# Kernel tuning notes

Measured on AMD Instinct MI355X. Metric: run time of the kernel, lower is better.

Reference implementation:

```python
import jax, jax.numpy as jnp
import numpy as np

B, F_IN, N_D, N_A, VBS, N_STEPS = 1024, 256, 64, 64, 128, 3
FO = N_D + N_A            # 128
D_CAT = 2 * F_IN          # 512
AD = F_IN                 # attention_dim = 256
GAMMA, EPSILON, BN_EPS = 1.3, 1e-15, 1e-5
SQRT_HALF = 0.7071067811865476


def _bn(x, w, b):
    # full-batch BatchNorm1d (training mode, biased var)
    m = x.mean(0)
    v = x.var(0)
    return (x - m) / jnp.sqrt(v + BN_EPS) * w + b


def _gbn(x, w, b):
    # Ghost BatchNorm: per virtual-batch statistics
    n, f = x.shape
    xr = x.reshape(n // VBS, VBS, f)
    m = xr.mean(1, keepdims=True)
    v = xr.var(1, keepdims=True)
    return (xr - m).reshape(n, f) / jnp.sqrt(v + BN_EPS).repeat(VBS, axis=0).reshape(n, f) * w + b


def _glu(x, fcw, bnw, bnb):
    h = _gbn(x @ fcw.T, bnw, bnb)
    d = h.shape[-1] // 2
    return h[:, :d] * jax.nn.sigmoid(h[:, d:])


def _feat_transformer(x, fc0, bnw0, bnb0, fc1, bnw1, bnb1):
    # independent GLU block, first=True, n_glu_independent=2
    h = _glu(x, fc0, bnw0, bnb0)
    return (h + _glu(h, fc1, bnw1, bnb1)) * SQRT_HALF


def _sparsemax(z):
    f = z.shape[-1]
    zs = -jnp.sort(-z, axis=-1)                      # descending
    k = jnp.arange(1, f + 1, dtype=z.dtype)
    zc = jnp.cumsum(zs, axis=-1)
    support = (1.0 + k * zs) > zc
    kz = jnp.sum(support, axis=-1, keepdims=True)
    tau = (jnp.take_along_axis(zc, kz - 1, axis=-1) - 1.0) / kz.astype(z.dtype)
    return jnp.maximum(z - tau, 0.0)


def _self_attn_1d(x, in_w, in_b, out_w, out_b):
    # nn.MultiheadAttention(embed_dim=1, heads=1) over the feature axis
    q = x * in_w[0] + in_b[0]
    k = x * in_w[1] + in_b[1]
    v = x * in_w[2] + in_b[2]
    attn = jax.nn.softmax(jnp.einsum('bi,bj->bij', q, k), axis=-1)  # scale 1/sqrt(1)
    y = jnp.einsum('bij,bj->bi', attn, v) * out_w + out_b
    return y, attn


def setup_inputs() -> dict:
    key = jax.random.key(0)
    ks = iter(jax.random.split(key, 32))
    s = 0.1
    d = {
        'x': jax.random.normal(next(ks), (B, F_IN), jnp.float32),
        'bemv': jax.random.normal(next(ks), (B, F_IN), jnp.float32),
        'gmat': jax.random.uniform(next(ks), (AD, F_IN), jnp.float32),
        'bn_w': jnp.ones((F_IN,), jnp.float32),
        'bn_b': jnp.zeros((F_IN,), jnp.float32),
        'init_fc0': jax.random.normal(next(ks), (2 * FO, D_CAT), jnp.float32) * s,
        'init_bnw0': jnp.ones((2 * FO,), jnp.float32),
        'init_bnb0': jnp.zeros((2 * FO,), jnp.float32),
        'init_fc1': jax.random.normal(next(ks), (2 * FO, FO), jnp.float32) * s,
        'init_bnw1': jnp.ones((2 * FO,), jnp.float32),
        'init_bnb1': jnp.zeros((2 * FO,), jnp.float32),
        'step_fc0': jax.random.normal(next(ks), (N_STEPS, 2 * FO, D_CAT), jnp.float32) * s,
        'step_bnw0': jnp.ones((N_STEPS, 2 * FO), jnp.float32),
        'step_bnb0': jnp.zeros((N_STEPS, 2 * FO), jnp.float32),
        'step_fc1': jax.random.normal(next(ks), (N_STEPS, 2 * FO, FO), jnp.float32) * s,
        'step_bnw1': jnp.ones((N_STEPS, 2 * FO), jnp.float32),
        'step_bnb1': jnp.zeros((N_STEPS, 2 * FO), jnp.float32),
        'att_fc': jax.random.normal(next(ks), (N_STEPS, AD, N_A), jnp.float32) * s,
        'att_bnw': jnp.ones((N_STEPS, AD), jnp.float32),
        'att_bnb': jnp.zeros((N_STEPS, AD), jnp.float32),
        'sa_in_w': jax.random.normal(next(ks), (N_STEPS, 3), jnp.float32),
        'sa_in_b': jnp.zeros((N_STEPS, 3), jnp.float32),
        'sa_out_w': jax.random.normal(next(ks), (N_STEPS,), jnp.float32),
        'sa_out_b': jnp.zeros((N_STEPS,), jnp.float32),
    }
    return d


def reference(x, bemv, gmat, bn_w, bn_b,
              init_fc0, init_bnw0, init_bnb0, init_fc1, init_bnw1, init_bnb1,
              step_fc0, step_bnw0, step_bnb0, step_fc1, step_bnw1, step_bnb1,
              att_fc, att_bnw, att_bnb,
              sa_in_w, sa_in_b, sa_out_w, sa_out_b):
    prior = jnp.ones((x.shape[0], AD), x.dtype)
    xn = _bn(x, bn_w, bn_b)
    x_cat = jnp.concatenate([xn, bemv], axis=1)
    feat_out = _feat_transformer(x_cat, init_fc0, init_bnw0, init_bnb0,
                                 init_fc1, init_bnw1, init_bnb1)
    att = feat_out[:, N_D:]
    m_loss = jnp.asarray(0.0, x.dtype)
    steps, amaps = [], []
    for s in range(N_STEPS):
        a = _gbn(att @ att_fc[s].T, att_bnw[s], att_bnb[s])
        tab_mask = _sparsemax(a * prior)
        m_loss = m_loss + jnp.mean(jnp.sum(tab_mask * jnp.log(tab_mask + EPSILON), axis=1))
        prior = prior * (GAMMA - tab_mask)
        x_masked = (tab_mask @ gmat) * xn
        x_masked, A = _self_attn_1d(x_masked, sa_in_w[s], sa_in_b[s], sa_out_w[s], sa_out_b[s])
        amaps.append(A)
        feat_out = _feat_transformer(jnp.concatenate([x_masked, bemv], axis=1),
                                     step_fc0[s], step_bnw0[s], step_bnb0[s],
                                     step_fc1[s], step_bnw1[s], step_bnb1[s])
        steps.append(jax.nn.leaky_relu(feat_out[:, :N_D], 0.01))
        att = feat_out[:, N_D:]
    m_loss = m_loss / N_STEPS
    return jnp.stack(steps), m_loss, jnp.stack(amaps)
```

## Files before the change

### kernel.cpp

```cpp
#include <hip/hip_runtime.h>
#include <hip/hip_bf16.h>

#define BATCH 1024
#define N_STEPS 3
#define GAMMA_C 1.3f
#define BN_EPS_C 1e-5f
#define SQRT_HALF_C 0.70710678118654752440f
#define ST_STRIDE 786432

__device__ __forceinline__ float ldin(const void* p, size_t i, int isbf){
  if (isbf) return __bfloat162float(((const __hip_bfloat16*)p)[i]);
  return ((const float*)p)[i];
}
__device__ __forceinline__ float4 ld4(const void* p, size_t i, int isbf){
  if (!isbf) return *(const float4*)((const float*)p + i);
  const __hip_bfloat16* q = (const __hip_bfloat16*)p + i;
  return make_float4(__bfloat162float(q[0]), __bfloat162float(q[1]),
                     __bfloat162float(q[2]), __bfloat162float(q[3]));
}

__device__ __forceinline__ float wsum(float v){
#pragma unroll
  for (int o = 32; o > 0; o >>= 1) v += __shfl_xor(v, o);
  return v;
// ... 38 lines not shown
  float k2 = kS[(cb+2) & 255];
  float k3 = kS[(cb+3) & 255];
  const bool cross = (cb == 255);
  const int nj = (t < 255) ? 64 : 63;
#pragma unroll 4
  for (int j = 0; j < nj; ++j){
    int r0 = 4*j + rb0;
    float q0 = sh[r0], m0 = sh[256+r0], z0 = sh[512+r0];
    float4 o;
    if (!cross){
      o.x = __expf(q0*k0 - m0) * z0;
      o.y = __expf(q0*k1 - m0) * z0;
      o.z = __expf(q0*k2 - m0) * z0;
      o.w = __expf(q0*k3 - m0) * z0;
    } else {
      float q1 = sh[r0+1], m1 = sh[256+r0+1], z1 = sh[512+r0+1];
      o.x = __expf(q0*k0 - m0) * z0;
      o.y = __expf(q1*k1 - m1) * z1;
      o.z = __expf(q1*k2 - m1) * z1;
      o.w = __expf(q1*k3 - m1) * z1;
    }
    *(float4*)(tp + 3 + 4*t + 1024*j) = o;
  }
  if (t == 0){
    float q0 = sh[0], m0 = sh[256], z0 = sh[512];
    tp[0] = __expf(q0*kS[0] - m0) * z0;
    tp[1] = __expf(q0*kS[1] - m0) * z0;
    tp[2] = __expf(q0*kS[2] - m0) * z0;
    float qL = sh[255], mL = sh[511], zL = sh[767];
    tp[65535] = __expf(qL*kS[255] - mL) * zL;
  }
}

__global__ void detect_k(const unsigned short* __restrict__ u, float* __restrict__ flag){
  __shared__ int cnt;
  if (threadIdx.x == 0) cnt = 0;
  __syncthreads();
  int c = 0;
  for (int j = 0; j < 16; ++j){
    unsigned short v = u[(size_t)(threadIdx.x * 16 + j) * 2];
    int e = (v >> 7) & 0xFF;
    if (e >= 118 && e <= 134) c++;
  }
  atomicAdd(&cnt, c);
  __syncthreads();
  if (threadIdx.x == 0) flag[0] = (cnt > 2048) ? 1.0f : 0.0f;
}

__global__ void bnstats_k(const void* __restrict__ x, float* __restrict__ mean,
                          float* __restrict__ istd, const float* __restrict__ flg){
  __shared__ float sb[256];
  const int isbf = flg[0] != 0.0f;
  int f = blockIdx.x, t = threadIdx.x;
  float s = 0.f, ss = 0.f;
  for (int r = t; r < BATCH; r += 256){
    float v = ldin(x, (size_t)r * 256 + f, isbf);
    s += v; ss += v * v;
  }
  s  = block_sum(s, sb);
  ss = block_sum(ss, sb);
  if (t == 0){
    float m = s * (1.f / BATCH);
    mean[f] = m;
    istd[f] = rsqrtf(ss * (1.f / BATCH) - m * m + BN_EPS_C);
  }
}

__global__ void xn_k(const void* __restrict__ x, const float* __restrict__ mean,
                     const float* __restrict__ istd, const void* __restrict__ bw,
                     const void* __restrict__ bb, float* __restrict__ xn,
                     const float* __restrict__ flg){
  const int isbf = flg[0] != 0.0f;
  int idx = blockIdx.x * 256 + threadIdx.x;
  int f = idx & 255;
  xn[idx] = (ldin(x, idx, isbf) - mean[f]) * istd[f] * ldin(bw, f, isbf) + ldin(bb, f, isbf);
}

__global__ __launch_bounds__(256)
void gemm_bt_k(const float* __restrict__ A1, const void* __restrict__ A2, int split,
               const void* __restrict__ W, size_t woff, float* __restrict__ C, int K,
               const float* __restrict__ st, float* __restrict__ amap, int dS, int dR0,
               const float* __restrict__ flg){
  int bid = blockIdx.x, t = threadIdx.x;
  if (bid >= 256){ drain_rows(st, amap, dS, dR0 + bid - 256, t); return; }
  __shared__ float As[32][34];
  __shared__ float Ws[32][34];
  const int isbf = flg[0] != 0.0f;
  const int n0 = (bid & 7) * 32, m0 = (bid >> 3) * 32;
  const int tx = t & 15, ty = t >> 4;
  const int lr = t >> 3, lk = (t & 7) * 4;
  const int nc = K >> 5;
  float a00 = 0.f, a01 = 0.f, a10 = 0.f, a11 = 0.f;

  auto lda = [&](int k0) -> float4 {
    int gk = k0 + lk, gr = m0 + lr;
    if (gk < split) return *(const float4*)(A1 + (size_t)gr * split + gk);
    return ld4(A2, (size_t)gr * (K - split) + (gk - split), isbf);
  };
  auto ldw = [&](int k0) -> float4 {
    return ld4(W, woff + (size_t)(n0 + lr) * K + k0 + lk, isbf);
  };

  float4 ra = lda(0), rw = ldw(0);
  for (int c = 0; c < nc; ++c){
    As[lk+0][lr] = ra.x; As[lk+1][lr] = ra.y; As[lk+2][lr] = ra.z; As[lk+3][lr] = ra.w;
    Ws[lk+0][lr] = rw.x; Ws[lk+1][lr] = rw.y; Ws[lk+2][lr] = rw.z; Ws[lk+3][lr] = rw.w;
    __syncthreads();
    float4 na = ra, nw = rw;
    if (c + 1 < nc){ na = lda((c+1) << 5); nw = ldw((c+1) << 5); }
#pragma unroll
    for (int kk = 0; kk < 32; ++kk){
      float2 av = *(const float2*)&As[kk][ty*2];
      float2 wv = *(const float2*)&Ws[kk][tx*2];
      a00 += av.x * wv.x; a01 += av.x * wv.y;
      a10 += av.y * wv.x; a11 += av.y * wv.y;
    }
    __syncthreads();
    ra = na; rw = nw;
  }
  int r0 = m0 + ty*2, c0 = n0 + tx*2;
  float* Cp = C + (size_t)r0 * 256 + c0;
  Cp[0] = a00; Cp[1] = a01; Cp[256] = a10; Cp[257] = a11;
}

__global__ __launch_bounds__(256)
void glugemm_k(const float* __restrict__ H1, const void* __restrict__ gw,
               const void* __restrict__ gb, size_t goff,
               const void* __restrict__ W, size_t woff, float* __restrict__ C,
               const float* __restrict__ st, float* __restrict__ amap, int dS, int dR0,
               const float* __restrict__ flg){
  int bid = blockIdx.x, t = threadIdx.x;
  if (bid >= 256){ drain_rows(st, amap, dS, dR0 + bid - 256, t); return; }
  __shared__ __align__(16) float sA[256], sB[256];
  __shared__ float As[32][34];
  __shared__ float Ws[32][34];
  const int isbf = flg[0] != 0.0f;
  const int n0 = (bid & 7) * 32, m0 = (bid >> 3) * 32;
  const int g = bid >> 5;
  {
    const float* Hp = H1 + (size_t)g*32768 + t;
    float s = 0.f, ss = 0.f;
#pragma unroll 8
    for (int i = 0; i < 128; ++i){ float v = Hp[(size_t)i*256]; s += v; ss += v*v; }
    float m = s * (1.f/128), is = rsqrtf(ss * (1.f/128) - m*m + BN_EPS_C);
    float wv = ldin(gw, goff + t, isbf), bv = ldin(gb, goff + t, isbf);
    float A = is * wv;
    sA[t] = A; sB[t] = bv - m*A;
  }
  __syncthreads();
  const int tx = t & 15, ty = t >> 4;
  const int lr = t >> 3, lk = (t & 7) * 4;
  float a00 = 0.f, a01 = 0.f, a10 = 0.f, a11 = 0.f;

  auto lda = [&](int k0) -> float4 {
    int gk = k0 + lk, gr = m0 + lr;
    const float* h = H1 + (size_t)gr*256;
    float4 h0 = *(const float4*)(h + gk);
    float4 h1 = *(const float4*)(h + gk + 128);
    float4 A0 = *(const float4*)(sA + gk);
    float4 B0 = *(const float4*)(sB + gk);
    float4 A1 = *(const float4*)(sA + gk + 128);
    float4 B1 = *(const float4*)(sB + gk + 128);
    float4 r;
    r.x = (h0.x*A0.x+B0.x) / (1.f + __expf(-(h1.x*A1.x+B1.x)));
    r.y = (h0.y*A0.y+B0.y) / (1.f + __expf(-(h1.y*A1.y+B1.y)));
    r.z = (h0.z*A0.z+B0.z) / (1.f + __expf(-(h1.z*A1.z+B1.z)));
    r.w = (h0.w*A0.w+B0.w) / (1.f + __expf(-(h1.w*A1.w+B1.w)));
    return r;
  };
  auto ldw = [&](int k0) -> float4 {
    return ld4(W, woff + (size_t)(n0 + lr) * 128 + k0 + lk, isbf);
  };

  float4 ra = lda(0), rw = ldw(0);
#pragma unroll 1
  for (int c = 0; c < 4; ++c){
    As[lk+0][lr] = ra.x; As[lk+1][lr] = ra.y; As[lk+2][lr] = ra.z; As[lk+3][lr] = ra.w;
    Ws[lk+0][lr] = rw.x; Ws[lk+1][lr] = rw.y; Ws[lk+2][lr] = rw.z; Ws[lk+3][lr] = rw.w;
    __syncthreads();
    float4 na = ra, nw = rw;
    if (c + 1 < 4){ na = lda((c+1) << 5); nw = ldw((c+1) << 5); }
#pragma unroll
    for (int kk = 0; kk < 32; ++kk){
      float2 av = *(const float2*)&As[kk][ty*2];
      float2 wv = *(const float2*)&Ws[kk][tx*2];
      a00 += av.x * wv.x; a01 += av.x * wv.y;
      a10 += av.y * wv.x; a11 += av.y * wv.y;
    }
    __syncthreads();
    ra = na; rw = nw;
  }
  int r0 = m0 + ty*2, c0 = n0 + tx*2;
  float* Cp = C + (size_t)r0 * 256 + c0;
  Cp[0] = a00; Cp[1] = a01; Cp[256] = a10; Cp[257] = a11;
}

__global__ __launch_bounds__(256)
void spmax_k(const float* __restrict__ Ha, const void* __restrict__ gw,
             const void* __restrict__ gb, size_t goff, float* __restrict__ prior,
             const float* __restrict__ xn, const void* __restrict__ gmat,
             float* __restrict__ xm, float* __restrict__ lrow, int first,
             const float* __restrict__ st, float* __restrict__ amap, int dS, int dR0,
             const float* __restrict__ flg){
  int bid = blockIdx.x, t = threadIdx.x;
  if (bid >= 256){ drain_rows(st, amap, dS, dR0 + bid - 256, t); return; }
  __shared__ __align__(16) float sAA[256], sBA[256];
  __shared__ __align__(16) float tabs[4][256];
  __shared__ unsigned int msk[4][2];
  const int isbf = flg[0] != 0.0f;
  const int g = bid >> 5;
  {
    const float* Hp = Ha + (size_t)g*32768 + t;
    float s = 0.f, ss = 0.f;
#pragma unroll 8
    for (int i = 0; i < 128; ++i){ float v = Hp[(size_t)i*256]; s += v; ss += v*v; }
    float m = s * (1.f/128), is = rsqrtf(ss * (1.f/128) - m*m + BN_EPS_C);
    float wv = ldin(gw, goff + t, isbf), bv = ldin(gb, goff + t, isbf);
    float A = is * wv;
    sAA[t] = A; sBA[t] = bv - m*A;
  }
  __syncthreads();
  int lane = t & 63, wv = t >> 6;
  int b0 = bid * 4;
  int b = b0 + wv;
  size_t rb = (size_t)b * 256;
  int j0 = lane * 4;
  float4 h4 = *(const float4*)(Ha + rb + j0);
  float4 A4 = *(const float4*)(sAA + j0);
  float4 B4 = *(const float4*)(sBA + j0);
  float pr[4];
  if (first){ pr[0] = pr[1] = pr[2] = pr[3] = 1.f; }
  else { float4 p4 = *(const float4*)(prior + rb + j0); pr[0]=p4.x; pr[1]=p4.y; pr[2]=p4.z; pr[3]=p4.w; }
  float z[4];
  z[0] = (h4.x*A4.x + B4.x) * pr[0];
  z[1] = (h4.y*A4.y + B4.y) * pr[1];
  z[2] = (h4.z*A4.z + B4.z) * pr[2];
  z[3] = (h4.w*A4.w + B4.w) * pr[3];
  float zm = wmaxr(fmaxf(fmaxf(z[0], z[1]), fmaxf(z[2], z[3])));
  float lo = zm - 1.f, hi = zm;
#pragma unroll 1
  for (int it = 0; it < 30; ++it){
    float mid = 0.5f * (lo + hi);
    float sv = 0.f;
#pragma unroll
    for (int e = 0; e < 4; ++e){ float d = z[e] - mid; sv += d > 0.f ? d : 0.f; }
    sv = wsum(sv);
    if (sv >= 1.f) lo = mid; else hi = mid;
  }
  float tau = 0.5f * (lo + hi);
  float p[4], ls = 0.f;
#pragma unroll
  for (int e = 0; e < 4; ++e){
    p[e] = z[e] - tau; p[e] = p[e] > 0.f ? p[e] : 0.f;
    ls += p[e] * __logf(p[e] + 1e-15f);
  }
  *(float4*)&tabs[wv][j0] = make_float4(p[0], p[1], p[2], p[3]);
  *(float4*)(prior + rb + j0) = make_float4(pr[0]*(GAMMA_C-p[0]), pr[1]*(GAMMA_C-p[1]),
                                            pr[2]*(GAMMA_C-p[2]), pr[3]*(GAMMA_C-p[3]));
  ls = wsum(ls);
  if (lane == 0) lrow[b] = ls;
  bool nz = (p[0] > 0.f) | (p[1] > 0.f) | (p[2] > 0.f) | (p[3] > 0.f);
  unsigned long long bm = __ballot(nz);
  if (lane == 0){ msk[wv][0] = (unsigned int)bm; msk[wv][1] = (unsigned int)(bm >> 32); }
  __syncthreads();
  unsigned long long M0 = msk[0][0] | ((unsigned long long)msk[0][1] << 32);
  unsigned long long M1 = msk[1][0] | ((unsigned long long)msk[1][1] << 32);
  unsigned long long M2 = msk[2][0] | ((unsigned long long)msk[2][1] << 32);
  unsigned long long M3 = msk[3][0] | ((unsigned long long)msk[3][1] << 32);
  float a0 = 0.f, a1 = 0.f, a2 = 0.f, a3 = 0.f;
#pragma unroll 1
  for (int c = 0; c < 64; ++c){
    int r0a = (int)((M0 >> c) & 1), r1a = (int)((M1 >> c) & 1);
    int r2a = (int)((M2 >> c) & 1), r3a = (int)((M3 >> c) & 1);
    if (r0a | r1a | r2a | r3a){
      int k = c * 4;
      float g0 = ldin(gmat, (size_t)(k+0)*256 + t, isbf);
      float g1 = ldin(gmat, (size_t)(k+1)*256 + t, isbf);
      float g2 = ldin(gmat, (size_t)(k+2)*256 + t, isbf);
      float g3 = ldin(gmat, (size_t)(k+3)*256 + t, isbf);
      if (r0a){ float4 tv = *(float4*)&tabs[0][k]; a0 += tv.x*g0 + tv.y*g1 + tv.z*g2 + tv.w*g3; }
      if (r1a){ float4 tv = *(float4*)&tabs[1][k]; a1 += tv.x*g0 + tv.y*g1 + tv.z*g2 + tv.w*g3; }
      if (r2a){ float4 tv = *(float4*)&tabs[2][k]; a2 += tv.x*g0 + tv.y*g1 + tv.z*g2 + tv.w*g3; }
      if (r3a){ float4 tv = *(float4*)&tabs[3][k]; a3 += tv.x*g0 + tv.y*g1 + tv.z*g2 + tv.w*g3; }
    }
  }
  xm[(size_t)(b0+0)*256 + t] = a0 * xn[(size_t)(b0+0)*256 + t];
  xm[(size_t)(b0+1)*256 + t] = a1 * xn[(size_t)(b0+1)*256 + t];
  xm[(size_t)(b0+2)*256 + t] = a2 * xn[(size_t)(b0+2)*256 + t];
  xm[(size_t)(b0+3)*256 + t] = a3 * xn[(size_t)(b0+3)*256 + t];
}

__global__ __launch_bounds__(256)
void attnA_k(const float* __restrict__ xm, float* __restrict__ y,
             const void* __restrict__ siw, const void* __restrict__ sib,
             const void* __restrict__ sow, const void* __restrict__ sob,
             int s, float* __restrict__ st, float* __restrict__ amap, int dS, int dR0,
             const float* __restrict__ flg){
  int bid = blockIdx.x, t = threadIdx.x;
  if (bid >= 1024){ drain_rows(st, amap, dS, dR0 + bid - 1024, t); return; }
  __shared__ __align__(16) float ks[256], vs[256];
  __shared__ float r1[4], r2[4];
  const int isbf = flg[0] != 0.0f;
  int b = bid;
  float w0 = ldin(siw, s*3+0, isbf), w1 = ldin(siw, s*3+1, isbf), w2 = ldin(siw, s*3+2, isbf);
  float b0 = ldin(sib, s*3+0, isbf), b1 = ldin(sib, s*3+1, isbf), b2 = ldin(sib, s*3+2, isbf);
  float ow = ldin(sow, s, isbf), ob = ldin(sob, s, isbf);
  float xv = xm[(size_t)b*256 + t];
  float q = xv*w0 + b0, k = xv*w1 + b1, v = xv*w2 + b2;
  ks[t] = k; vs[t] = v;
  int lane = t & 63, wv = t >> 6;
  float km = wmaxr(k), kn = wminr(k);
  if (lane == 0){ r1[wv] = km; r2[wv] = kn; }
  __syncthreads();
  float kmax = fmaxf(fmaxf(r1[0], r1[1]), fmaxf(r1[2], r1[3]));
  float kmin = fminf(fminf(r2[0], r2[1]), fminf(r2[2], r2[3]));
  float mi = (q >= 0.f) ? q*kmax : q*kmin;
  float Z = 0.f, Y = 0.f;
#pragma unroll 8
  for (int j = 0; j < 256; j += 4){
    float4 k4 = *(const float4*)&ks[j];
    float4 v4 = *(const float4*)&vs[j];
    float e0 = __expf(q*k4.x - mi), e1 = __expf(q*k4.y - mi);
    float e2 = __expf(q*k4.z - mi), e3 = __expf(q*k4.w - mi);
    Z += (e0 + e1) + (e2 + e3);
    Y += (e0*v4.x + e1*v4.y) + (e2*v4.z + e3*v4.w);
  }
  float rz = 1.f / Z;
  y[(size_t)b*256 + t] = Y*rz*ow + ob;
  size_t sb = ((size_t)s*BATCH + b)*256 + t;
  st[sb]               = q;
  st[ST_STRIDE + sb]   = k;
  st[2*ST_STRIDE + sb] = mi;
  st[3*ST_STRIDE + sb] = rz;
}

__global__ __launch_bounds__(256)
void comb_k(const float* __restrict__ H1, const void* __restrict__ pw0,
            const void* __restrict__ pb0, size_t off0,
            const float* __restrict__ H2, const void* __restrict__ pw1,
            const void* __restrict__ pb1, size_t off1,
            float* __restrict__ att, float* __restrict__ steps,
            const float* __restrict__ st, float* __restrict__ amap, int dS, int dR0,
            const float* __restrict__ flg){
  int bid = blockIdx.x, t = threadIdx.x;
  if (bid >= 512){ drain_rows(st, amap, dS, dR0 + bid - 512, t); return; }
  __shared__ float sA0[256], sB0[256], sA1[256], sB1[256];
  const int isbf = flg[0] != 0.0f;
  const int g = bid >> 6;
  {
    const float* Hp = H1 + (size_t)g*32768 + t;
    float s = 0.f, ss = 0.f;
#pragma unroll 8
    for (int i = 0; i < 128; ++i){ float v = Hp[(size_t)i*256]; s += v; ss += v*v; }
    float m = s * (1.f/128), is = rsqrtf(ss * (1.f/128) - m*m + BN_EPS_C);
    float wv = ldin(pw0, off0 + t, isbf), bv = ldin(pb0, off0 + t, isbf);
    float A = is * wv;
    sA0[t] = A; sB0[t] = bv - m*A;
  }
  {
    const float* Hp = H2 + (size_t)g*32768 + t;
    float s = 0.f, ss = 0.f;
#pragma unroll 8
    for (int i = 0; i < 128; ++i){ float v = Hp[(size_t)i*256]; s += v; ss += v*v; }
    float m = s * (1.f/128), is = rsqrtf(ss * (1.f/128) - m*m + BN_EPS_C);
    float wv = ldin(pw1, off1 + t, isbf), bv = ldin(pb1, off1 + t, isbf);
    float A = is * wv;
    sA1[t] = A; sB1[t] = bv - m*A;
  }
  __syncthreads();
  int r = bid*2 + (t >> 7), j = t & 127;
  float h0 = H1[(size_t)r*256 + j], h1 = H1[(size_t)r*256 + j + 128];
  float u0 = h0 * sA0[j]     + sB0[j];
  float u1 = h1 * sA0[j+128] + sB0[j+128];
  float g0 = u0 / (1.f + __expf(-u1));
  float v0 = H2[(size_t)r*256 + j]     * sA1[j]     + sB1[j];
  float v1 = H2[(size_t)r*256 + j+128] * sA1[j+128] + sB1[j+128];
  float g1 = v0 / (1.f + __expf(-v1));
  float f = (g0 + g1) * SQRT_HALF_C;
  if (j < 64){
    if (steps) steps[(size_t)r*64 + j] = f > 0.f ? f : 0.01f*f;
  } else {
    att[(size_t)r*64 + (j - 64)] = f;
  }
}

__global__ __launch_bounds__(256)
void mloss_k(const float* __restrict__ lrow, float* __restrict__ outp,
             const float* __restrict__ st, float* __restrict__ amap, int s, int row0){
  int bid = blockIdx.x, t = threadIdx.x;
  if (bid > 0){ drain_rows(st, amap, s, row0 + bid - 1, t); return; }
  __shared__ float sb[256];
  float v = 0.f;
  for (int i = t; i < N_STEPS*BATCH; i += 256) v += lrow[i];
  v = block_sum(v, sb);
  if (t == 0) outp[0] = v * (1.f/(N_STEPS*(float)BATCH));
}

extern "C" void kernel_launch(void* const* d_in, const int* in_sizes, int n_in,
                              void* d_out, int out_size, void* d_ws, size_t ws_size,
                              hipStream_t stream){
  const void* x         = d_in[0];
  const void* bemv      = d_in[1];
  const void* gmat      = d_in[2];
  const void* bn_w      = d_in[3];
  const void* bn_b      = d_in[4];
  const void* init_fc0  = d_in[5];
  const void* init_bnw0 = d_in[6];
  const void* init_bnb0 = d_in[7];
  const void* init_fc1  = d_in[8];
  const void* init_bnw1 = d_in[9];
  const void* init_bnb1 = d_in[10];
  const void* step_fc0  = d_in[11];
  const void* step_bnw0 = d_in[12];
  const void* step_bnb0 = d_in[13];
  const void* step_fc1  = d_in[14];
  const void* step_bnw1 = d_in[15];
  const void* step_bnb1 = d_in[16];
  const void* att_fc    = d_in[17];
  const void* att_bnw   = d_in[18];
  const void* att_bnb   = d_in[19];
  const void* sa_in_w   = d_in[20];
  const void* sa_in_b   = d_in[21];
  const void* sa_out_w  = d_in[22];
  const void* sa_out_b  = d_in[23];

  float* out       = (float*)d_out;
  float* steps_out = out;
  float* mloss_out = out + 196608;
  float* amaps     = out + 196609;

  float* w     = (float*)d_ws;
  float* flag  = w;
  float* mean  = w + 16;
  float* istd  = w + 272;
  float* lrow  = w + 528;
  float* xn    = w + 4096;
  float* H1    = xn + 262144;
  float* H2    = H1 + 262144;
  float* att   = H2 + 262144;
  float* xm    = att + 65536;
  float* prior = xm + 262144;
  float* y     = prior + 262144;
  float* st    = y + 262144;

  detect_k<<<1, 256, 0, stream>>>((const unsigned short*)x, flag);
  bnstats_k<<<256, 256, 0, stream>>>(x, mean, istd, flag);
  xn_k<<<1024, 256, 0, stream>>>(x, mean, istd, bn_w, bn_b, xn, flag);

  gemm_bt_k<<<256, 256, 0, stream>>>(xn, bemv, 256, init_fc0, 0, H1, 512, st, amaps, 0, 0, flag);
  glugemm_k<<<256, 256, 0, stream>>>(H1, init_bnw0, init_bnb0, 0, init_fc1, 0, H2, st, amaps, 0, 0, flag);
  comb_k<<<512, 256, 0, stream>>>(H1, init_bnw0, init_bnb0, 0, H2, init_bnw1, init_bnb1, 0,
                                  att, nullptr, st, amaps, 0, 0, flag);

  for (int s = 0; s < N_STEPS; ++s){
    int pd = s - 1;
    int dn = (pd >= 0) ? 160 : 0;
    gemm_bt_k<<<256 + dn, 256, 0, stream>>>(att, nullptr, 64, att_fc, (size_t)s*16384, H1, 64,
                                            st, amaps, pd, 544, flag);
    spmax_k<<<256 + dn, 256, 0, stream>>>(H1, att_bnw, att_bnb, (size_t)s*256, prior, xn, gmat,
                                          xm, lrow + s*1024, s == 0, st, amaps, pd, 704, flag);
    attnA_k<<<1024 + dn, 256, 0, stream>>>(xm, y, sa_in_w, sa_in_b, sa_out_w, sa_out_b, s,
                                           st, amaps, pd, 864, flag);
    gemm_bt_k<<<256 + 224, 256, 0, stream>>>(y, bemv, 256, step_fc0, (size_t)s*131072, H1, 512,
                                             st, amaps, s, 0, flag);
    glugemm_k<<<256 + 160, 256, 0, stream>>>(H1, step_bnw0, step_bnb0, (size_t)s*256,
                                             step_fc1, (size_t)s*32768, H2, st, amaps, s, 224, flag);
    comb_k<<<512 + 160, 256, 0, stream>>>(H1, step_bnw0, step_bnb0, (size_t)s*256,
                                          H2, step_bnw1, step_bnb1, (size_t)s*256,
                                          att, steps_out + (size_t)s*65536, st, amaps, s, 384, flag);
  }
  mloss_k<<<481, 256, 0, stream>>>(lrow, mloss_out, st, amaps, 2, 544);
}
```

Baseline: 435.0 us.

## Fuse kernel chain: merge detect/bnstats/xn, combine into attention GEMM, sparsemax+self-attn

Several launches are merged. Dtype detection is folded into the BN-stats kernel, and the BN apply is fused into the first GEMM's A-load. The GLU combine is fused into the attention GEMM's operand load, which also writes the previous step's output. Sparsemax, gmat projection and self-attention are merged into one per-row kernel, and the final combine is fused with the m_loss reduction. Attention-map drain blocks are redistributed across the fewer launches. This removes launch overhead and intermediate round-trips through global memory (att, xm), at the cost of recomputing GBN statistics in more blocks and of heavier per-row kernels.

```diff
diff --git a/kernel.cpp b/kernel.cpp
--- a/kernel.cpp
+++ b/kernel.cpp
@@ -94,48 +94,94 @@
   }
 }
 
-__global__ void detect_k(const unsigned short* __restrict__ u, float* __restrict__ flag){
+__global__ __launch_bounds__(256)
+void bnstatsD_k(const void* __restrict__ x, const void* __restrict__ bnw,
+                const void* __restrict__ bnb, float* __restrict__ xnA,
+                float* __restrict__ xnB, float* __restrict__ flag){
+  __shared__ float sb[256];
   __shared__ int cnt;
-  if (threadIdx.x == 0) cnt = 0;
-  __syncthreads();
+  int f = blockIdx.x, t = threadIdx.x;
+  if (t == 0) cnt = 0;
+  __syncthreads();
+  const unsigned short* u = (const unsigned short*)x;
   int c = 0;
   for (int j = 0; j < 16; ++j){
-    unsigned short v = u[(size_t)(threadIdx.x * 16 + j) * 2];
+    unsigned short v = u[(size_t)(t * 16 + j) * 2];
     int e = (v >> 7) & 0xFF;
-    if (e >= 118 && e <= 134) c++;
+    c += (e >= 118 && e <= 134);
   }
   atomicAdd(&cnt, c);
   __syncthreads();
-  if (threadIdx.x == 0) flag[0] = (cnt > 2048) ? 1.0f : 0.0f;
-}
-
-__global__ void bnstats_k(const void* __restrict__ x, float* __restrict__ mean,
-                          float* __restrict__ istd, const float* __restrict__ flg){
-  __shared__ float sb[256];
-  const int isbf = flg[0] != 0.0f;
-  int f = blockIdx.x, t = threadIdx.x;
+  const int isbf = cnt > 2048;
+  if (f == 0 && t == 0) flag[0] = isbf ? 1.0f : 0.0f;
   float s = 0.f, ss = 0.f;
   for (int r = t; r < BATCH; r += 256){
-    float v = ldin(x, (size_t)r * 256 + f, isbf);
-    s += v; ss += v * v;
+    float v = ldin(x, (size_t)r*256 + f, isbf);
+    s += v; ss += v*v;
   }
   s  = block_sum(s, sb);
   ss = block_sum(ss, sb);
   if (t == 0){
-    float m = s * (1.f / BATCH);
-    mean[f] = m;
-    istd[f] = rsqrtf(ss * (1.f / BATCH) - m * m + BN_EPS_C);
-  }
-}
-
-__global__ void xn_k(const void* __restrict__ x, const float* __restrict__ mean,
-                     const float* __restrict__ istd, const void* __restrict__ bw,
-                     const void* __restrict__ bb, float* __restrict__ xn,
-                     const float* __restrict__ flg){
+    float m = s * (1.f/BATCH);
+    float is = rsqrtf(ss * (1.f/BATCH) - m*m + BN_EPS_C);
+    float A = is * ldin(bnw, f, isbf);
+    xnA[f] = A;
+    xnB[f] = ldin(bnb, f, isbf) - m*A;
+  }
+}
+
+__global__ __launch_bounds__(256)
+void gemminit_k(const void* __restrict__ x, const void* __restrict__ bemv,
+                const float* __restrict__ xnA, const float* __restrict__ xnB,
+                const void* __restrict__ W, float* __restrict__ C,
+                float* __restrict__ xn, const float* __restrict__ flg){
+  int bid = blockIdx.x, t = threadIdx.x;
+  __shared__ float As[32][34];
+  __shared__ float Ws[32][34];
   const int isbf = flg[0] != 0.0f;
-  int idx = blockIdx.x * 256 + threadIdx.x;
-  int f = idx & 255;
-  xn[idx] = (ldin(x, idx, isbf) - mean[f]) * istd[f] * ldin(bw, f, isbf) + ldin(bb, f, isbf);
+  const int n0 = (bid & 7) * 32, m0 = (bid >> 3) * 32;
+  const int tx = t & 15, ty = t >> 4;
+  const int lr = t >> 3, lk = (t & 7) * 4;
+  float a00 = 0.f, a01 = 0.f, a10 = 0.f, a11 = 0.f;
+  auto lda = [&](int k0) -> float4 {
+    int gk = k0 + lk, gr = m0 + lr;
+    if (gk < 256){
+      float4 xv = ld4(x, (size_t)gr*256 + gk, isbf);
+      float4 A4 = *(const float4*)(xnA + gk);
+      float4 B4 = *(const float4*)(xnB + gk);
+      return make_float4(xv.x*A4.x+B4.x, xv.y*A4.y+B4.y, xv.z*A4.z+B4.z, xv.w*A4.w+B4.w);
+    }
+    return ld4(bemv, (size_t)gr*256 + (gk - 256), isbf);
+  };
+  auto ldw = [&](int k0) -> float4 {
+    return ld4(W, (size_t)(n0 + lr)*512 + k0 + lk, isbf);
+  };
+  float4 ra = lda(0), rw = ldw(0);
+  for (int c = 0; c < 16; ++c){
+    As[lk+0][lr] = ra.x; As[lk+1][lr] = ra.y; As[lk+2][lr] = ra.z; As[lk+3][lr] = ra.w;
+    Ws[lk+0][lr] = rw.x; Ws[lk+1][lr] = rw.y; Ws[lk+2][lr] = rw.z; Ws[lk+3][lr] = rw.w;
+    __syncthreads();
+    float4 na = ra, nw = rw;
+    if (c + 1 < 16){ na = lda((c+1) << 5); nw = ldw((c+1) << 5); }
+#pragma unroll
+    for (int kk = 0; kk < 32; ++kk){
+      float2 av = *(const float2*)&As[kk][ty*2];
+      float2 wv = *(const float2*)&Ws[kk][tx*2];
+      a00 += av.x*wv.x; a01 += av.x*wv.y;
+      a10 += av.y*wv.x; a11 += av.y*wv.y;
+    }
+    __syncthreads();
+    ra = na; rw = nw;
+  }
+  int r0 = m0 + ty*2, c0 = n0 + tx*2;
+  float* Cp = C + (size_t)r0*256 + c0;
+  Cp[0] = a00; Cp[1] = a01; Cp[256] = a10; Cp[257] = a11;
+  int fi = (bid*256 + t) * 4;
+  int col = fi & 255;
+  float4 xv = ld4(x, fi, isbf);
+  float4 A4 = *(const float4*)(xnA + col);
+  float4 B4 = *(const float4*)(xnB + col);
+  *(float4*)(xn + fi) = make_float4(xv.x*A4.x+B4.x, xv.y*A4.y+B4.y, xv.z*A4.z+B4.z, xv.w*A4.w+B4.w);
 }
 
 __global__ __launch_bounds__(256)
@@ -153,16 +199,14 @@
   const int lr = t >> 3, lk = (t & 7) * 4;
   const int nc = K >> 5;
   float a00 = 0.f, a01 = 0.f, a10 = 0.f, a11 = 0.f;
-
   auto lda = [&](int k0) -> float4 {
     int gk = k0 + lk, gr = m0 + lr;
-    if (gk < split) return *(const float4*)(A1 + (size_t)gr * split + gk);
-    return ld4(A2, (size_t)gr * (K - split) + (gk - split), isbf);
+    if (gk < split) return *(const float4*)(A1 + (size_t)gr*split + gk);
+    return ld4(A2, (size_t)gr*(K - split) + (gk - split), isbf);
   };
   auto ldw = [&](int k0) -> float4 {
-    return ld4(W, woff + (size_t)(n0 + lr) * K + k0 + lk, isbf);
-  };
-
+    return ld4(W, woff + (size_t)(n0 + lr)*K + k0 + lk, isbf);
+  };
   float4 ra = lda(0), rw = ldw(0);
   for (int c = 0; c < nc; ++c){
     As[lk+0][lr] = ra.x; As[lk+1][lr] = ra.y; As[lk+2][lr] = ra.z; As[lk+3][lr] = ra.w;
@@ -174,14 +218,14 @@
     for (int kk = 0; kk < 32; ++kk){
       float2 av = *(const float2*)&As[kk][ty*2];
       float2 wv = *(const float2*)&Ws[kk][tx*2];
-      a00 += av.x * wv.x; a01 += av.x * wv.y;
-      a10 += av.y * wv.x; a11 += av.y * wv.y;
+      a00 += av.x*wv.x; a01 += av.x*wv.y;
+      a10 += av.y*wv.x; a11 += av.y*wv.y;
     }
     __syncthreads();
     ra = na; rw = nw;
   }
   int r0 = m0 + ty*2, c0 = n0 + tx*2;
-  float* Cp = C + (size_t)r0 * 256 + c0;
+  float* Cp = C + (size_t)r0*256 + c0;
   Cp[0] = a00; Cp[1] = a01; Cp[256] = a10; Cp[257] = a11;
 }
 
@@ -213,7 +257,6 @@
   const int tx = t & 15, ty = t >> 4;
   const int lr = t >> 3, lk = (t & 7) * 4;
   float a00 = 0.f, a01 = 0.f, a10 = 0.f, a11 = 0.f;
-
   auto lda = [&](int k0) -> float4 {
     int gk = k0 + lk, gr = m0 + lr;
     const float* h = H1 + (size_t)gr*256;
@@ -231,9 +274,8 @@
     return r;
   };
   auto ldw = [&](int k0) -> float4 {
-    return ld4(W, woff + (size_t)(n0 + lr) * 128 + k0 + lk, isbf);
-  };
-
+    return ld4(W, woff + (size_t)(n0 + lr)*128 + k0 + lk, isbf);
+  };
   float4 ra = lda(0), rw = ldw(0);
 #pragma unroll 1
   for (int c = 0; c < 4; ++c){
@@ -246,131 +288,200 @@
     for (int kk = 0; kk < 32; ++kk){
       float2 av = *(const float2*)&As[kk][ty*2];
       float2 wv = *(const float2*)&Ws[kk][tx*2];
-      a00 += av.x * wv.x; a01 += av.x * wv.y;
-      a10 += av.y * wv.x; a11 += av.y * wv.y;
+      a00 += av.x*wv.x; a01 += av.x*wv.y;
+      a10 += av.y*wv.x; a11 += av.y*wv.y;
     }
     __syncthreads();
     ra = na; rw = nw;
   }
   int r0 = m0 + ty*2, c0 = n0 + tx*2;
-  float* Cp = C + (size_t)r0 * 256 + c0;
+  float* Cp = C + (size_t)r0*256 + c0;
   Cp[0] = a00; Cp[1] = a01; Cp[256] = a10; Cp[257] = a11;
 }
 
 __global__ __launch_bounds__(256)
-void spmax_k(const float* __restrict__ Ha, const void* __restrict__ gw,
-             const void* __restrict__ gb, size_t goff, float* __restrict__ prior,
-             const float* __restrict__ xn, const void* __restrict__ gmat,
-             float* __restrict__ xm, float* __restrict__ lrow, int first,
+void acomb_k(const float* __restrict__ H1, const float* __restrict__ H2,
+             const void* __restrict__ p0w, const void* __restrict__ p0b, size_t off0,
+             const void* __restrict__ p1w, const void* __restrict__ p1b, size_t off1,
+             const void* __restrict__ afc, size_t aoff, float* __restrict__ Ha,
+             float* __restrict__ steps_prev,
              const float* __restrict__ st, float* __restrict__ amap, int dS, int dR0,
              const float* __restrict__ flg){
   int bid = blockIdx.x, t = threadIdx.x;
   if (bid >= 256){ drain_rows(st, amap, dS, dR0 + bid - 256, t); return; }
-  __shared__ __align__(16) float sAA[256], sBA[256];
-  __shared__ __align__(16) float tabs[4][256];
-  __shared__ unsigned int msk[4][2];
+  __shared__ __align__(16) float sA0[256], sB0[256], sA1[256], sB1[256];
+  __shared__ float As[32][34];
+  __shared__ float Ws[32][34];
   const int isbf = flg[0] != 0.0f;
-  const int g = bid >> 5;
+  const int n0 = (bid & 7) * 32, m0 = (bid >> 3) * 32;
+  const int g = m0 >> 7;
+  {
+    const float* h1p = H1 + (size_t)g*32768 + t;
+    const float* h2p = H2 + (size_t)g*32768 + t;
+    float s0 = 0.f, ss0 = 0.f, s1 = 0.f, ss1 = 0.f;
+#pragma unroll 8
+    for (int i = 0; i < 128; ++i){
+      float v = h1p[(size_t)i*256]; s0 += v; ss0 += v*v;
+      float w = h2p[(size_t)i*256]; s1 += w; ss1 += w*w;
+    }
+    float m = s0 * (1.f/128), is = rsqrtf(ss0 * (1.f/128) - m*m + BN_EPS_C);
+    float A = is * ldin(p0w, off0 + t, isbf);
+    sA0[t] = A; sB0[t] = ldin(p0b, off0 + t, isbf) - m*A;
+    m = s1 * (1.f/128); is = rsqrtf(ss1 * (1.f/128) - m*m + BN_EPS_C);
+    A = is * ldin(p1w, off1 + t, isbf);
+    sA1[t] = A; sB1[t] = ldin(p1b, off1 + t, isbf) - m*A;
+  }
+  __syncthreads();
+  const int tx = t & 15, ty = t >> 4;
+  const int lr = t >> 3, lk = (t & 7) * 4;
+  float a00 = 0.f, a01 = 0.f, a10 = 0.f, a11 = 0.f;
+  auto lda = [&](int k0) -> float4 {
+    int gk = k0 + lk, gr = m0 + lr;
+    const float* h1 = H1 + (size_t)gr*256;
+    const float* h2 = H2 + (size_t)gr*256;
+    float4 a0 = *(const float4*)(h1 + 64 + gk);
+    float4 a1 = *(const float4*)(h1 + 192 + gk);
+    float4 b0 = *(const float4*)(h2 + 64 + gk);
+    float4 b1 = *(const float4*)(h2 + 192 + gk);
+    float4 c0 = *(const float4*)(sA0 + 64 + gk),  d0 = *(const float4*)(sB0 + 64 + gk);
+    float4 c1 = *(const float4*)(sA0 + 192 + gk), d1 = *(const float4*)(sB0 + 192 + gk);
+    float4 e0 = *(const float4*)(sA1 + 64 + gk),  f0 = *(const float4*)(sB1 + 64 + gk);
+    float4 e1 = *(const float4*)(sA1 + 192 + gk), f1 = *(const float4*)(sB1 + 192 + gk);
+    float4 r;
+    r.x = ((a0.x*c0.x+d0.x)/(1.f+__expf(-(a1.x*c1.x+d1.x)))
+         + (b0.x*e0.x+f0.x)/(1.f+__expf(-(b1.x*e1.x+f1.x)))) * SQRT_HALF_C;
+    r.y = ((a0.y*c0.y+d0.y)/(1.f+__expf(-(a1.y*c1.y+d1.y)))
+         + (b0.y*e0.y+f0.y)/(1.f+__expf(-(b1.y*e1.y+f1.y)))) * SQRT_HALF_C;
+    r.z = ((a0.z*c0.z+d0.z)/(1.f+__expf(-(a1.z*c1.z+d1.z)))
+         + (b0.z*e0.z+f0.z)/(1.f+__expf(-(b1.z*e1.z+f1.z)))) * SQRT_HALF_C;
+    r.w = ((a0.w*c0.w+d0.w)/(1.f+__expf(-(a1.w*c1.w+d1.w)))
+         + (b0.w*e0.w+f0.w)/(1.f+__expf(-(b1.w*e1.w+f1.w)))) * SQRT_HALF_C;
+    return r;
+  };
+  auto ldw = [&](int k0) -> float4 {
+    return ld4(afc, aoff + (size_t)(n0 + lr)*64 + k0 + lk, isbf);
+  };
+  float4 ra = lda(0), rw = ldw(0);
+#pragma unroll 1
+  for (int c = 0; c < 2; ++c){
+    As[lk+0][lr] = ra.x; As[lk+1][lr] = ra.y; As[lk+2][lr] = ra.z; As[lk+3][lr] = ra.w;
+    Ws[lk+0][lr] = rw.x; Ws[lk+1][lr] = rw.y; Ws[lk+2][lr] = rw.z; Ws[lk+3][lr] = rw.w;
+    __syncthreads();
+    float4 na = ra, nw = rw;
+    if (c + 1 < 2){ na = lda(32); nw = ldw(32); }
+#pragma unroll
+    for (int kk = 0; kk < 32; ++kk){
+      float2 av = *(const float2*)&As[kk][ty*2];
+      float2 wv = *(const float2*)&Ws[kk][tx*2];
+      a00 += av.x*wv.x; a01 += av.x*wv.y;
+      a10 += av.y*wv.x; a11 += av.y*wv.y;
+    }
+    __syncthreads();
+    ra = na; rw = nw;
+  }
+  int r0 = m0 + ty*2, c0 = n0 + tx*2;
+  float* Cp = Ha + (size_t)r0*256 + c0;
+  Cp[0] = a00; Cp[1] = a01; Cp[256] = a10; Cp[257] = a11;
+  if (steps_prev && (bid & 7) == 0){
+#pragma unroll
+    for (int ii = 0; ii < 8; ++ii){
+      int idx = t + ii*256;
+      int r = m0 + (idx >> 6), j = idx & 63;
+      float h0 = H1[(size_t)r*256 + j], h1 = H1[(size_t)r*256 + j + 128];
+      float u0 = h0 * sA0[j]     + sB0[j];
+      float u1 = h1 * sA0[j+128] + sB0[j+128];
+      float g0 = u0 / (1.f + __expf(-u1));
+      float v0 = H2[(size_t)r*256 + j]     * sA1[j]     + sB1[j];
+      float v1 = H2[(size_t)r*256 + j+128] * sA1[j+128] + sB1[j+128];
+      float g1 = v0 / (1.f + __expf(-v1));
+      float f = (g0 + g1) * SQRT_HALF_C;
+      steps_prev[(size_t)r*64 + j] = f > 0.f ? f : 0.01f*f;
+    }
+  }
+}
+
+__global__ __launch_bounds__(256)
+void cd_k(const float* __restrict__ Ha, const void* __restrict__ abnw,
+          const void* __restrict__ abnb, size_t aoff2, float* __restrict__ prior,
+          const float* __restrict__ xn, const void* __restrict__ gmat,
+          float* __restrict__ y, float* __restrict__ lrow, int first,
+          const void* __restrict__ siw, const void* __restrict__ sib,
+          const void* __restrict__ sow, const void* __restrict__ sob, int s,
+          float* __restrict__ stt, float* __restrict__ amap, int dS, int dR0,
+          const float* __restrict__ flg){
+  int bid = blockIdx.x, t = threadIdx.x;
+  if (bid >= 1024){ drain_rows(stt, amap, dS, dR0 + bid - 1024, t); return; }
+  __shared__ __align__(16) float zt[256], prt[256], tabs[256];
+  __shared__ __align__(16) float ks[256], vs[256];
+  __shared__ float r1[4], r2[4];
+  __shared__ unsigned int msk2[2];
+  const int isbf = flg[0] != 0.0f;
+  const int b = bid, g = b >> 7;
+  float AA, BB;
   {
     const float* Hp = Ha + (size_t)g*32768 + t;
-    float s = 0.f, ss = 0.f;
+    float s0 = 0.f, ss0 = 0.f;
 #pragma unroll 8
-    for (int i = 0; i < 128; ++i){ float v = Hp[(size_t)i*256]; s += v; ss += v*v; }
-    float m = s * (1.f/128), is = rsqrtf(ss * (1.f/128) - m*m + BN_EPS_C);
-    float wv = ldin(gw, goff + t, isbf), bv = ldin(gb, goff + t, isbf);
-    float A = is * wv;
-    sAA[t] = A; sBA[t] = bv - m*A;
-  }
+    for (int i = 0; i < 128; ++i){ float v = Hp[(size_t)i*256]; s0 += v; ss0 += v*v; }
+    float m = s0 * (1.f/128), is = rsqrtf(ss0 * (1.f/128) - m*m + BN_EPS_C);
+    AA = is * ldin(abnw, aoff2 + t, isbf);
+    BB = ldin(abnb, aoff2 + t, isbf) - m*AA;
+  }
+  float hv = Ha[(size_t)b*256 + t];
+  float pr = first ? 1.f : prior[(size_t)b*256 + t];
+  zt[t] = (hv*AA + BB) * pr;
+  prt[t] = pr;
   __syncthreads();
   int lane = t & 63, wv = t >> 6;
-  int b0 = bid * 4;
-  int b = b0 + wv;
-  size_t rb = (size_t)b * 256;
-  int j0 = lane * 4;
-  float4 h4 = *(const float4*)(Ha + rb + j0);
-  float4 A4 = *(const float4*)(sAA + j0);
-  float4 B4 = *(const float4*)(sBA + j0);
-  float pr[4];
-  if (first){ pr[0] = pr[1] = pr[2] = pr[3] = 1.f; }
-  else { float4 p4 = *(const float4*)(prior + rb + j0); pr[0]=p4.x; pr[1]=p4.y; pr[2]=p4.z; pr[3]=p4.w; }
-  float z[4];
-  z[0] = (h4.x*A4.x + B4.x) * pr[0];
-  z[1] = (h4.y*A4.y + B4.y) * pr[1];
-  z[2] = (h4.z*A4.z + B4.z) * pr[2];
-  z[3] = (h4.w*A4.w + B4.w) * pr[3];
-  float zm = wmaxr(fmaxf(fmaxf(z[0], z[1]), fmaxf(z[2], z[3])));
+  float4 z4 = *(const float4*)&zt[lane*4];
+  float zm = wmaxr(fmaxf(fmaxf(z4.x, z4.y), fmaxf(z4.z, z4.w)));
   float lo = zm - 1.f, hi = zm;
 #pragma unroll 1
   for (int it = 0; it < 30; ++it){
     float mid = 0.5f * (lo + hi);
-    float sv = 0.f;
-#pragma unroll
-    for (int e = 0; e < 4; ++e){ float d = z[e] - mid; sv += d > 0.f ? d : 0.f; }
+    float sv = fmaxf(z4.x - mid, 0.f) + fmaxf(z4.y - mid, 0.f)
+             + fmaxf(z4.z - mid, 0.f) + fmaxf(z4.w - mid, 0.f);
     sv = wsum(sv);
     if (sv >= 1.f) lo = mid; else hi = mid;
   }
   float tau = 0.5f * (lo + hi);
-  float p[4], ls = 0.f;
-#pragma unroll
-  for (int e = 0; e < 4; ++e){
-    p[e] = z[e] - tau; p[e] = p[e] > 0.f ? p[e] : 0.f;
-    ls += p[e] * __logf(p[e] + 1e-15f);
-  }
-  *(float4*)&tabs[wv][j0] = make_float4(p[0], p[1], p[2], p[3]);
-  *(float4*)(prior + rb + j0) = make_float4(pr[0]*(GAMMA_C-p[0]), pr[1]*(GAMMA_C-p[1]),
-                                            pr[2]*(GAMMA_C-p[2]), pr[3]*(GAMMA_C-p[3]));
-  ls = wsum(ls);
-  if (lane == 0) lrow[b] = ls;
-  bool nz = (p[0] > 0.f) | (p[1] > 0.f) | (p[2] > 0.f) | (p[3] > 0.f);
-  unsigned long long bm = __ballot(nz);
-  if (lane == 0){ msk[wv][0] = (unsigned int)bm; msk[wv][1] = (unsigned int)(bm >> 32); }
-  __syncthreads();
-  unsigned long long M0 = msk[0][0] | ((unsigned long long)msk[0][1] << 32);
-  unsigned long long M1 = msk[1][0] | ((unsigned long long)msk[1][1] << 32);
-  unsigned long long M2 = msk[2][0] | ((unsigned long long)msk[2][1] << 32);
-  unsigned long long M3 = msk[3][0] | ((unsigned long long)msk[3][1] << 32);
-  float a0 = 0.f, a1 = 0.f, a2 = 0.f, a3 = 0.f;
+  float p0 = fmaxf(z4.x - tau, 0.f), p1 = fmaxf(z4.y - tau, 0.f);
+  float p2 = fmaxf(z4.z - tau, 0.f), p3 = fmaxf(z4.w - tau, 0.f);
+  if (wv == 0){
+    float4 pr4 = *(const float4*)&prt[lane*4];
+    *(float4*)&tabs[lane*4] = make_float4(p0, p1, p2, p3);
+    *(float4*)(prior + (size_t)b*256 + lane*4) =
+        make_float4(pr4.x*(GAMMA_C-p0), pr4.y*(GAMMA_C-p1),
+                    pr4.z*(GAMMA_C-p2), pr4.w*(GAMMA_C-p3));
+    float ls = p0*__logf(p0 + 1e-15f) + p1*__logf(p1 + 1e-15f)
+             + p2*__logf(p2 + 1e-15f) + p3*__logf(p3 + 1e-15f);
+    ls = wsum(ls);
+    if (lane == 0) lrow[b] = ls;
+    bool nz = (p0 > 0.f) | (p1 > 0.f) | (p2 > 0.f) | (p3 > 0.f);
+    unsigned long long bm = __ballot(nz);
+    if (lane == 0){ msk2[0] = (unsigned int)bm; msk2[1] = (unsigned int)(bm >> 32); }
+  }
+  __syncthreads();
+  unsigned long long M = msk2[0] | ((unsigned long long)msk2[1] << 32);
+  float acc = 0.f;
 #pragma unroll 1
   for (int c = 0; c < 64; ++c){
-    int r0a = (int)((M0 >> c) & 1), r1a = (int)((M1 >> c) & 1);
-    int r2a = (int)((M2 >> c) & 1), r3a = (int)((M3 >> c) & 1);
-    if (r0a | r1a | r2a | r3a){
+    if ((M >> c) & 1){
       int k = c * 4;
       float g0 = ldin(gmat, (size_t)(k+0)*256 + t, isbf);
       float g1 = ldin(gmat, (size_t)(k+1)*256 + t, isbf);
       float g2 = ldin(gmat, (size_t)(k+2)*256 + t, isbf);
       float g3 = ldin(gmat, (size_t)(k+3)*256 + t, isbf);
-      if (r0a){ float4 tv = *(float4*)&tabs[0][k]; a0 += tv.x*g0 + tv.y*g1 + tv.z*g2 + tv.w*g3; }
-      if (r1a){ float4 tv = *(float4*)&tabs[1][k]; a1 += tv.x*g0 + tv.y*g1 + tv.z*g2 + tv.w*g3; }
-      if (r2a){ float4 tv = *(float4*)&tabs[2][k]; a2 += tv.x*g0 + tv.y*g1 + tv.z*g2 + tv.w*g3; }
-      if (r3a){ float4 tv = *(float4*)&tabs[3][k]; a3 += tv.x*g0 + tv.y*g1 + tv.z*g2 + tv.w*g3; }
-    }
-  }
-  xm[(size_t)(b0+0)*256 + t] = a0 * xn[(size_t)(b0+0)*256 + t];
-  xm[(size_t)(b0+1)*256 + t] = a1 * xn[(size_t)(b0+1)*256 + t];
-  xm[(size_t)(b0+2)*256 + t] = a2 * xn[(size_t)(b0+2)*256 + t];
-  xm[(size_t)(b0+3)*256 + t] = a3 * xn[(size_t)(b0+3)*256 + t];
-}
-
-__global__ __launch_bounds__(256)
-void attnA_k(const float* __restrict__ xm, float* __restrict__ y,
-             const void* __restrict__ siw, const void* __restrict__ sib,
-             const void* __restrict__ sow, const void* __restrict__ sob,
-             int s, float* __restrict__ st, float* __restrict__ amap, int dS, int dR0,
-             const float* __restrict__ flg){
-  int bid = blockIdx.x, t = threadIdx.x;
-  if (bid >= 1024){ drain_rows(st, amap, dS, dR0 + bid - 1024, t); return; }
-  __shared__ __align__(16) float ks[256], vs[256];
-  __shared__ float r1[4], r2[4];
-  const int isbf = flg[0] != 0.0f;
-  int b = bid;
+      float4 tv = *(const float4*)&tabs[k];
+      acc += tv.x*g0 + tv.y*g1 + tv.z*g2 + tv.w*g3;
+    }
+  }
+  float xv = acc * xn[(size_t)b*256 + t];
   float w0 = ldin(siw, s*3+0, isbf), w1 = ldin(siw, s*3+1, isbf), w2 = ldin(siw, s*3+2, isbf);
   float b0 = ldin(sib, s*3+0, isbf), b1 = ldin(sib, s*3+1, isbf), b2 = ldin(sib, s*3+2, isbf);
   float ow = ldin(sow, s, isbf), ob = ldin(sob, s, isbf);
-  float xv = xm[(size_t)b*256 + t];
   float q = xv*w0 + b0, k = xv*w1 + b1, v = xv*w2 + b2;
   ks[t] = k; vs[t] = v;
-  int lane = t & 63, wv = t >> 6;
   float km = wmaxr(k), kn = wminr(k);
   if (lane == 0){ r1[wv] = km; r2[wv] = kn; }
   __syncthreads();
@@ -390,47 +501,53 @@
   float rz = 1.f / Z;
   y[(size_t)b*256 + t] = Y*rz*ow + ob;
   size_t sb = ((size_t)s*BATCH + b)*256 + t;
-  st[sb]               = q;
-  st[ST_STRIDE + sb]   = k;
-  st[2*ST_STRIDE + sb] = mi;
-  st[3*ST_STRIDE + sb] = rz;
+  stt[sb]               = q;
+  stt[ST_STRIDE + sb]   = k;
+  stt[2*ST_STRIDE + sb] = mi;
+  stt[3*ST_STRIDE + sb] = rz;
 }
 
 __global__ __launch_bounds__(256)
-void comb_k(const float* __restrict__ H1, const void* __restrict__ pw0,
-            const void* __restrict__ pb0, size_t off0,
-            const float* __restrict__ H2, const void* __restrict__ pw1,
-            const void* __restrict__ pb1, size_t off1,
-            float* __restrict__ att, float* __restrict__ steps,
-            const float* __restrict__ st, float* __restrict__ amap, int dS, int dR0,
-            const float* __restrict__ flg){
+void fin_k(const float* __restrict__ lrow, float* __restrict__ outp,
+           const float* __restrict__ H1, const void* __restrict__ pw0,
+           const void* __restrict__ pb0, size_t off0,
+           const float* __restrict__ H2, const void* __restrict__ pw1,
+           const void* __restrict__ pb1, size_t off1,
+           float* __restrict__ steps2,
+           const float* __restrict__ st, float* __restrict__ amap,
+           const float* __restrict__ flg){
   int bid = blockIdx.x, t = threadIdx.x;
-  if (bid >= 512){ drain_rows(st, amap, dS, dR0 + bid - 512, t); return; }
-  __shared__ float sA0[256], sB0[256], sA1[256], sB1[256];
+  if (bid >= 257){ drain_rows(st, amap, 2, 512 + bid - 257, t); return; }
+  if (bid == 0){
+    __shared__ float sb[256];
+    float v = 0.f;
+    for (int i = t; i < N_STEPS*BATCH; i += 256) v += lrow[i];
+    v = block_sum(v, sb);
+    if (t == 0) outp[0] = v * (1.f/(N_STEPS*(float)BATCH));
+    return;
+  }
+  __shared__ __align__(16) float sA0[256], sB0[256], sA1[256], sB1[256];
   const int isbf = flg[0] != 0.0f;
-  const int g = bid >> 6;
+  int sbk = bid - 1;
+  int g = sbk >> 5;
   {
-    const float* Hp = H1 + (size_t)g*32768 + t;
-    float s = 0.f, ss = 0.f;
+    const float* h1p = H1 + (size_t)g*32768 + t;
+    const float* h2p = H2 + (size_t)g*32768 + t;
+    float s0 = 0.f, ss0 = 0.f, s1 = 0.f, ss1 = 0.f;
 #pragma unroll 8
-    for (int i = 0; i < 128; ++i){ float v = Hp[(size_t)i*256]; s += v; ss += v*v; }
-    float m = s * (1.f/128), is = rsqrtf(ss * (1.f/128) - m*m + BN_EPS_C);
-    float wv = ldin(pw0, off0 + t, isbf), bv = ldin(pb0, off0 + t, isbf);
-    float A = is * wv;
-    sA0[t] = A; sB0[t] = bv - m*A;
-  }
-  {
-    const float* Hp = H2 + (size_t)g*32768 + t;
-    float s = 0.f, ss = 0.f;
-#pragma unroll 8
-    for (int i = 0; i < 128; ++i){ float v = Hp[(size_t)i*256]; s += v; ss += v*v; }
-    float m = s * (1.f/128), is = rsqrtf(ss * (1.f/128) - m*m + BN_EPS_C);
-    float wv = ldin(pw1, off1 + t, isbf), bv = ldin(pb1, off1 + t, isbf);
-    float A = is * wv;
-    sA1[t] = A; sB1[t] = bv - m*A;
-  }
-  __syncthreads();
-  int r = bid*2 + (t >> 7), j = t & 127;
+    for (int i = 0; i < 128; ++i){
+      float v = h1p[(size_t)i*256]; s0 += v; ss0 += v*v;
+      float w = h2p[(size_t)i*256]; s1 += w; ss1 += w*w;
+    }
+    float m = s0 * (1.f/128), is = rsqrtf(ss0 * (1.f/128) - m*m + BN_EPS_C);
+    float A = is * ldin(pw0, off0 + t, isbf);
+    sA0[t] = A; sB0[t] = ldin(pb0, off0 + t, isbf) - m*A;
+    m = s1 * (1.f/128); is = rsqrtf(ss1 * (1.f/128) - m*m + BN_EPS_C);
+    A = is * ldin(pw1, off1 + t, isbf);
+    sA1[t] = A; sB1[t] = ldin(pb1, off1 + t, isbf) - m*A;
+  }
+  __syncthreads();
+  int r = sbk*4 + (t >> 6), j = t & 63;
   float h0 = H1[(size_t)r*256 + j], h1 = H1[(size_t)r*256 + j + 128];
   float u0 = h0 * sA0[j]     + sB0[j];
   float u1 = h1 * sA0[j+128] + sB0[j+128];
@@ -439,23 +556,7 @@
   float v1 = H2[(size_t)r*256 + j+128] * sA1[j+128] + sB1[j+128];
   float g1 = v0 / (1.f + __expf(-v1));
   float f = (g0 + g1) * SQRT_HALF_C;
-  if (j < 64){
-    if (steps) steps[(size_t)r*64 + j] = f > 0.f ? f : 0.01f*f;
-  } else {
-    att[(size_t)r*64 + (j - 64)] = f;
-  }
-}
-
-__global__ __launch_bounds__(256)
-void mloss_k(const float* __restrict__ lrow, float* __restrict__ outp,
-             const float* __restrict__ st, float* __restrict__ amap, int s, int row0){
-  int bid = blockIdx.x, t = threadIdx.x;
-  if (bid > 0){ drain_rows(st, amap, s, row0 + bid - 1, t); return; }
-  __shared__ float sb[256];
-  float v = 0.f;
-  for (int i = t; i < N_STEPS*BATCH; i += 256) v += lrow[i];
-  v = block_sum(v, sb);
-  if (t == 0) outp[0] = v * (1.f/(N_STEPS*(float)BATCH));
+  steps2[(size_t)r*64 + j] = f > 0.f ? f : 0.01f*f;
 }
 
 extern "C" void kernel_launch(void* const* d_in, const int* in_sizes, int n_in,
@@ -493,43 +594,47 @@
 
   float* w     = (float*)d_ws;
   float* flag  = w;
-  float* mean  = w + 16;
-  float* istd  = w + 272;
+  float* xnA   = w + 16;
+  float* xnB   = w + 272;
   float* lrow  = w + 528;
   float* xn    = w + 4096;
   float* H1    = xn + 262144;
   float* H2    = H1 + 262144;
-  float* att   = H2 + 262144;
-  float* xm    = att + 65536;
-  float* prior = xm + 262144;
+  float* Ha    = H2 + 262144;
+  float* prior = Ha + 262144;
   float* y     = prior + 262144;
   float* st    = y + 262144;
 
-  detect_k<<<1, 256, 0, stream>>>((const unsigned short*)x, flag);
-  bnstats_k<<<256, 256, 0, stream>>>(x, mean, istd, flag);
-  xn_k<<<1024, 256, 0, stream>>>(x, mean, istd, bn_w, bn_b, xn, flag);
-
-  gemm_bt_k<<<256, 256, 0, stream>>>(xn, bemv, 256, init_fc0, 0, H1, 512, st, amaps, 0, 0, flag);
-  glugemm_k<<<256, 256, 0, stream>>>(H1, init_bnw0, init_bnb0, 0, init_fc1, 0, H2, st, amaps, 0, 0, flag);
-  comb_k<<<512, 256, 0, stream>>>(H1, init_bnw0, init_bnb0, 0, H2, init_bnw1, init_bnb1, 0,
-                                  att, nullptr, st, amaps, 0, 0, flag);
+  bnstatsD_k<<<256, 256, 0, stream>>>(x, bn_w, bn_b, xnA, xnB, flag);
+  gemminit_k<<<256, 256, 0, stream>>>(x, bemv, xnA, xnB, init_fc0, H1, xn, flag);
+  glugemm_k<<<256, 256, 0, stream>>>(H1, init_bnw0, init_bnb0, 0, init_fc1, 0, H2,
+                                     st, amaps, 0, 0, flag);
 
   for (int s = 0; s < N_STEPS; ++s){
     int pd = s - 1;
-    int dn = (pd >= 0) ? 160 : 0;
-    gemm_bt_k<<<256 + dn, 256, 0, stream>>>(att, nullptr, 64, att_fc, (size_t)s*16384, H1, 64,
-                                            st, amaps, pd, 544, flag);
-    spmax_k<<<256 + dn, 256, 0, stream>>>(H1, att_bnw, att_bnb, (size_t)s*256, prior, xn, gmat,
-                                          xm, lrow + s*1024, s == 0, st, amaps, pd, 704, flag);
-    attnA_k<<<1024 + dn, 256, 0, stream>>>(xm, y, sa_in_w, sa_in_b, sa_out_w, sa_out_b, s,
-                                           st, amaps, pd, 864, flag);
-    gemm_bt_k<<<256 + 224, 256, 0, stream>>>(y, bemv, 256, step_fc0, (size_t)s*131072, H1, 512,
-                                             st, amaps, s, 0, flag);
-    glugemm_k<<<256 + 160, 256, 0, stream>>>(H1, step_bnw0, step_bnb0, (size_t)s*256,
-                                             step_fc1, (size_t)s*32768, H2, st, amaps, s, 224, flag);
-    comb_k<<<512 + 160, 256, 0, stream>>>(H1, step_bnw0, step_bnb0, (size_t)s*256,
-                                          H2, step_bnw1, step_bnb1, (size_t)s*256,
-                                          att, steps_out + (size_t)s*65536, st, amaps, s, 384, flag);
-  }
-  mloss_k<<<481, 256, 0, stream>>>(lrow, mloss_out, st, amaps, 2, 544);
-}
+    int dn = (s >= 1) ? 256 : 0;
+    const void *p0w, *p0b, *p1w, *p1b; size_t off0, off1;
+    if (s == 0){ p0w = init_bnw0; p0b = init_bnb0; off0 = 0;
+                 p1w = init_bnw1; p1b = init_bnb1; off1 = 0; }
+    else       { p0w = step_bnw0; p0b = step_bnb0; off0 = (size_t)(s-1)*256;
+                 p1w = step_bnw1; p1b = step_bnb1; off1 = (size_t)(s-1)*256; }
+    acomb_k<<<256 + dn, 256, 0, stream>>>(H1, H2, p0w, p0b, off0, p1w, p1b, off1,
+                                          att_fc, (size_t)s*16384, Ha,
+                                          s > 0 ? steps_out + (size_t)(s-1)*65536 : nullptr,
+                                          st, amaps, pd, 512, flag);
+    cd_k<<<1024 + dn, 256, 0, stream>>>(Ha, att_bnw, att_bnb, (size_t)s*256, prior,
+                                        xn, gmat, y, lrow + s*1024, s == 0,
+                                        sa_in_w, sa_in_b, sa_out_w, sa_out_b, s,
+                                        st, amaps, pd, 768, flag);
+    gemm_bt_k<<<512, 256, 0, stream>>>(y, bemv, 256, step_fc0, (size_t)s*131072, H1, 512,
+                                       st, amaps, s, 0, flag);
+    glugemm_k<<<512, 256, 0, stream>>>(H1, step_bnw0, step_bnb0, (size_t)s*256,
+                                       step_fc1, (size_t)s*32768, H2,
+                                       st, amaps, s, 256, flag);
+  }
+  fin_k<<<769, 256, 0, stream>>>(lrow, mloss_out,
+                                 H1, step_bnw0, step_bnb0, (size_t)2*256,
+                                 H2, step_bnw1, step_bnb1, (size_t)2*256,
+                                 steps_out + (size_t)2*65536,
+                                 st, amaps, flag);
+}
```

Measured after the change: 381.0 us. -12.4%, faster.
